# Kernel tuning notes

Measured on AMD Instinct MI355X. Metric: run time of the kernel, lower is better.

## Reference

```python
import jax, jax.numpy as jnp
import numpy as np

HEADS = 4
BN_EPS = 1e-5


def _linear_attention(x, heads):
    # x: [B, L, C]; per-head linear attention: softmax(Q,dim=feat) @ (softmax(K,dim=seq)^T @ V)
    B, L, C = x.shape
    dh = C // heads
    h = x.reshape(B, L, heads, dh)
    q = jax.nn.softmax(h, axis=-1)          # softmax over feature dim (dim=2 in torch)
    k = jax.nn.softmax(h, axis=1)           # softmax over sequence dim (dim=1 in torch)
    kv = jnp.einsum('blhd,blhe->bhde', k, h)   # [B, H, dh, dh]
    out = jnp.einsum('blhd,bhde->blhe', q, kv) # [B, L, H, dh]
    return out.reshape(B, L, C)


def setup_inputs() -> dict:
    key = jax.random.key(0)
    ks = jax.random.split(key, 10)
    B, C, L, DOUT, NB = 32, 32, 16384, 10, 3
    s = 0.1
    return {
        'x': jax.random.normal(ks[0], (B, C, L), jnp.float32),
        'fcW1': jax.random.normal(ks[1], (NB, C, C), jnp.float32) * s,
        'fcb1': jax.random.normal(ks[2], (NB, C), jnp.float32) * s,
        'fcW2': jax.random.normal(ks[3], (NB, C, C), jnp.float32) * s,
        'fcb2': jax.random.normal(ks[4], (NB, C), jnp.float32) * s,
        'Wh': jax.random.normal(ks[5], (C, C), jnp.float32) * s,
        'bh': jax.random.normal(ks[6], (C,), jnp.float32) * s,
        'bn_gamma': jnp.ones((C,), jnp.float32),
        'bn_beta': jnp.zeros((C,), jnp.float32),
        'bn_mean': jnp.zeros((C,), jnp.float32),
        'bn_var': jnp.ones((C,), jnp.float32),
        'Wf': jax.random.normal(ks[7], (C, DOUT), jnp.float32) * s,
        'bf': jax.random.normal(ks[8], (DOUT,), jnp.float32) * s,
    }


def reference(x, fcW1, fcb1, fcW2, fcb2, Wh, bh, bn_gamma, bn_beta, bn_mean, bn_var, Wf, bf):
    gelu = lambda t: jax.nn.gelu(t, approximate=False)  # torch default GELU is exact erf
    h = jnp.transpose(x, (0, 2, 1))  # [B, C, L] -> [B, L, C]
    n_blocks = fcW1.shape[0]
    for i in range(n_blocks):
        h = _linear_attention(h, HEADS)
        h = gelu(h @ fcW1[i] + fcb1[i])
        h = gelu(h @ fcW2[i] + fcb2[i])
    pooled = jnp.mean(h, axis=1)  # AdaptiveAvgPool1d(1) over L -> [B, C]
    y = pooled @ Wh + bh
    y = (y - bn_mean) * jax.lax.rsqrt(bn_var + BN_EPS) * bn_gamma + bn_beta  # BatchNorm1d (eval)
    y = gelu(y)
    return y @ Wf + bf
```

## Files before the change

### kernel.cpp

```cpp
#include <hip/hip_runtime.h>
#include <cstddef>

#define B_ 32
#define C_ 32
#define L_ 16384
#define H_ 4
#define DH_ 8
#define NB_ 3
#define DOUT_ 10
#define SEG_ 256
#define S_ (L_/SEG_)

#define TILE 256
#define AST  40
#define OST  260

typedef _Float16 f16_t;
typedef _Float16 f16x2 __attribute__((ext_vector_type(2)));
typedef _Float16 f16x8 __attribute__((ext_vector_type(8)));
typedef float    f32x4 __attribute__((ext_vector_type(4)));

__device__ __forceinline__ float gelu_f(float x){
    const float z  = fabsf(x) * 0.70710678118654752440f;
    const float t  = __builtin_amdgcn_rcpf(fmaf(0.3275911f, z, 1.0f));
    const float e  = __expf(-z * z);
    float p = fmaf(t, 1.061405429f, -1.453152027f);
    p = fmaf(t, p, 1.421413741f);
    p = fmaf(t, p, -0.284496736f);
    p = fmaf(t, p, 0.254829592f);
    const float erfz = 1.0f - p * t * e;
    const float phi  = fmaf(copysignf(erfz, x), 0.5f, 0.5f);
    return x * phi;
}

__global__ __launch_bounds__(256) void stats_kernel(const float* __restrict__ h,
                                                    float* __restrict__ part){
    const int seg = blockIdx.x;
    const int hd  = blockIdx.y;
    const int b   = blockIdx.z;
    const int t   = threadIdx.x;
    const int d   = t >> 5;
    const int j   = t & 31;

    __shared__ float tile[8][SEG_];
    __shared__ float sm[8];

    const float* hb = h + (size_t)b * ((size_t)C_*L_) + (size_t)(hd*DH_)*L_ + (size_t)seg*SEG_;

    for (int f = t; f < 8*SEG_/4; f += 256){
        const int row = f >> 6;
        const int c4  = (f & 63) << 2;
        *(f32x4*)&tile[row][c4] = *(const f32x4*)&hb[(size_t)row*L_ + c4];
    }
    __syncthreads();

    float m = -INFINITY;
    #pragma unroll
    for (int i = 0; i < SEG_/32; i++) m = fmaxf(m, tile[d][j + 32*i]);
    m = fmaxf(m, __shfl_xor(m, 1));
    m = fmaxf(m, __shfl_xor(m, 2));
    m = fmaxf(m, __shfl_xor(m, 4));
    m = fmaxf(m, __shfl_xor(m, 8));
    m = fmaxf(m, __shfl_xor(m, 16));
    if (j == 0) sm[d] = m;
    const float m_d = m;

    float s = 0.0f;
    float kv[8];
    #pragma unroll
    for (int e = 0; e < 8; e++) kv[e] = 0.0f;
    #pragma unroll
    for (int i = 0; i < SEG_/32; i++){
        const int k = j + 32*i;
        const float ek = __expf(tile[d][k] - m_d);
        s += ek;
        #pragma unroll
        for (int e = 0; e < 8; e++) kv[e] = fmaf(ek, tile[e][k], kv[e]);
    }
    s += __shfl_xor(s, 1);  s += __shfl_xor(s, 2);  s += __shfl_xor(s, 4);
    s += __shfl_xor(s, 8);  s += __shfl_xor(s, 16);
    #pragma unroll
    for (int e = 0; e < 8; e++){
        kv[e] += __shfl_xor(kv[e], 1);  kv[e] += __shfl_xor(kv[e], 2);
        kv[e] += __shfl_xor(kv[e], 4);  kv[e] += __shfl_xor(kv[e], 8);
        kv[e] += __shfl_xor(kv[e], 16);
    }
    __syncthreads();

    float* po = part + (size_t)((b*H_ + hd)*S_ + seg) * 80;
    if (j == 0){
        po[8 + d] = s;
        #pragma unroll
        for (int e = 0; e < 8; e++) po[16 + d*8 + e] = kv[e];
    }
    if (t < 8) po[t] = sm[t];
}

__global__ __launch_bounds__(64) void merge_kernel(const float* __restrict__ part,
                                                   float* __restrict__ kvn){
    const int bh = blockIdx.x;
    const int t  = threadIdx.x;
    const int d  = t >> 3;
    const float* p = part + (size_t)bh * S_ * 80;
    float M = -INFINITY;
    for (int s2 = 0; s2 < S_; s2++) M = fmaxf(M, p[s2*80 + d]);
    float ssum = 0.0f, kvsum = 0.0f;
    for (int s2 = 0; s2 < S_; s2++){
        float sc = __expf(p[s2*80 + d] - M);
        ssum  += p[s2*80 + 8  + d] * sc;
        kvsum += p[s2*80 + 16 + t] * sc;
    }
    kvn[(size_t)bh*64 + t] = kvsum / ssum;
}

template<bool LAST>
__global__ __launch_bounds__(256)
__attribute__((amdgpu_waves_per_eu(3, 4)))
void block_kernel(const float* hin,
                  float* hout,
                  const float* __restrict__ kvn,
                  const float* __restrict__ W1,
                  const float* __restrict__ b1,
                  const float* __restrict__ W2,
                  const float* __restrict__ b2,
                  float* __restrict__ part_out,
                  float* __restrict__ pooled){
    __shared__ __align__(16) char uni[TILE*AST*2];
    f16_t* Ash = (f16_t*)uni;
    float* O16 = (float*)uni;
    __shared__ f16_t Bsh1[32*AST];
    __shared__ f16_t Bsh2[32*AST];
    __shared__ float sb1[32], sb2[32];
    __shared__ float pool[32];

    const int tid = threadIdx.x;
    const int b   = blockIdx.y;
    const int l0  = blockIdx.x * TILE;
    const int l   = l0 + tid;
    const size_t base = (size_t)b * ((size_t)C_*L_);
    const float* kv = kvn + (size_t)b * (H_*DH_*DH_);

    for (int i = tid; i < 1024; i += 256){
        const int k = i >> 5, n = i & 31;
        Bsh1[n*AST + k] = (f16_t)W1[i];
        Bsh2[n*AST + k] = (f16_t)W2[i];
    }
    if (tid < 32){ sb1[tid] = b1[tid]; sb2[tid] = b2[tid]; }
    if (LAST && tid < 32) pool[tid] = 0.0f;

    float h[32];
    #pragma unroll
    for (int c = 0; c < 32; c++) h[c] = hin[base + (size_t)c*L_ + l];

    float attn[32];
    #pragma unroll
    for (int hh = 0; hh < 4; hh++){
        float mq = h[hh*8];
        #pragma unroll
        for (int d2 = 1; d2 < 8; d2++) mq = fmaxf(mq, h[hh*8 + d2]);
        float es[8]; float qs = 0.f;
        #pragma unroll
        for (int d2 = 0; d2 < 8; d2++){ es[d2] = __expf(h[hh*8 + d2] - mq); qs += es[d2]; }
        const float inv = __builtin_amdgcn_rcpf(qs);
        #pragma unroll
        for (int e = 0; e < 8; e++){
            float a = 0.f;
            #pragma unroll
            for (int d2 = 0; d2 < 8; d2++) a += es[d2] * kv[hh*64 + d2*8 + e];
            attn[hh*8 + e] = a * inv;
        }
    }

    #pragma unroll
    for (int k2 = 0; k2 < 32; k2 += 2){
        f16x2 pr = { (f16_t)attn[k2], (f16_t)attn[k2+1] };
        *(f16x2*)&Ash[tid*AST + k2] = pr;
    }
    __syncthreads();

    const int wv   = tid >> 6;
    const int lane = tid & 63;
    const int lr   = lane & 15;
    const int lk   = lane >> 4;
    const f32x4 zero = {0.f, 0.f, 0.f, 0.f};

    f16x8 a[4], bw[2];
    f32x4 d[8];

    #pragma unroll
    for (int mt = 0; mt < 4; mt++)
        a[mt] = *(const f16x8*)&Ash[(wv*64 + mt*16 + lr)*AST + lk*8];
    #pragma unroll
    for (int nt = 0; nt < 2; nt++)
        bw[nt] = *(const f16x8*)&Bsh1[(nt*16 + lr)*AST + lk*8];
    #pragma unroll
    for (int nt = 0; nt < 2; nt++)
        #pragma unroll
        for (int mt = 0; mt < 4; mt++)
            d[nt*4+mt] = __builtin_amdgcn_mfma_f32_16x16x32_f16(a[mt], bw[nt], zero, 0, 0, 0);

    #pragma unroll
    for (int nt = 0; nt < 2; nt++){
        const float bias = sb1[nt*16 + lr];
        #pragma unroll
        for (int mt = 0; mt < 4; mt++){
            #pragma unroll
            for (int r = 0; r < 4; r++){
                const float v = gelu_f(d[nt*4+mt][r] + bias);
                Ash[(wv*64 + mt*16 + lk*4 + r)*AST + (nt*16 + lr)] = (f16_t)v;
            }
        }
    }
    __syncthreads();

    #pragma unroll
    for (int mt = 0; mt < 4; mt++)
        a[mt] = *(const f16x8*)&Ash[(wv*64 + mt*16 + lr)*AST + lk*8];
    #pragma unroll
    for (int nt = 0; nt < 2; nt++)
        bw[nt] = *(const f16x8*)&Bsh2[(nt*16 + lr)*AST + lk*8];
    #pragma unroll
    for (int nt = 0; nt < 2; nt++)
        #pragma unroll
        for (int mt = 0; mt < 4; mt++)
            d[nt*4+mt] = __builtin_amdgcn_mfma_f32_16x16x32_f16(a[mt], bw[nt], zero, 0, 0, 0);

    #pragma unroll
    for (int nt = 0; nt < 2; nt++){
        const float bias = sb2[nt*16 + lr];
        #pragma unroll
        for (int mt = 0; mt < 4; mt++)
            #pragma unroll
            for (int r = 0; r < 4; r++)
                d[nt*4+mt][r] = gelu_f(d[nt*4+mt][r] + bias);
    }

    if (!LAST){
        const int row16 = tid >> 4;
        const int grp   = tid & 15;
        #pragma unroll
        for (int nt = 0; nt < 2; nt++){
            __syncthreads();
            #pragma unroll
            for (int mt = 0; mt < 4; mt++)
                *(f32x4*)&O16[lr*OST + wv*64 + mt*16 + lk*4] = d[nt*4+mt];
            __syncthreads();
            #pragma unroll
            for (int c = 0; c < 16; c++)
                hout[base + (size_t)(nt*16 + c)*L_ + l0 + tid] = O16[c*OST + tid];

            const int head = nt*2 + (row16 >> 3);
            const int dd   = row16 & 7;
            const float* rowD = &O16[row16*OST];
            const float* rowE = &O16[(row16 & 8)*OST];
            float m = -INFINITY;
            #pragma unroll
            for (int i = 0; i < 16; i++) m = fmaxf(m, rowD[grp + 16*i]);
            m = fmaxf(m, __shfl_xor(m, 1)); m = fmaxf(m, __shfl_xor(m, 2));
            m = fmaxf(m, __shfl_xor(m, 4)); m = fmaxf(m, __shfl_xor(m, 8));
            float s = 0.f, kvp[8];
            #pragma unroll
            for (int e = 0; e < 8; e++) kvp[e] = 0.f;
            #pragma unroll
            for (int i = 0; i < 16; i++){
                const int k = grp + 16*i;
                const float ek = __expf(rowD[k] - m);
                s += ek;
                #pragma unroll
                for (int e = 0; e < 8; e++) kvp[e] = fmaf(ek, rowE[e*OST + k], kvp[e]);
            }
            s += __shfl_xor(s, 1); s += __shfl_xor(s, 2);
            s += __shfl_xor(s, 4); s += __shfl_xor(s, 8);
            #pragma unroll
            for (int e = 0; e < 8; e++){
                kvp[e] += __shfl_xor(kvp[e], 1); kvp[e] += __shfl_xor(kvp[e], 2);
                kvp[e] += __shfl_xor(kvp[e], 4); kvp[e] += __shfl_xor(kvp[e], 8);
            }
            if (grp == 0){
                float* po = part_out + (size_t)((b*H_ + head)*S_ + blockIdx.x) * 80;
                po[dd]     = m;
                po[8 + dd] = s;
                #pragma unroll
                for (int e = 0; e < 8; e++) po[16 + dd*8 + e] = kvp[e];
            }
        }
    } else {
        __syncthreads();
        #pragma unroll
        for (int nt = 0; nt < 2; nt++){
            float ps = 0.f;
            #pragma unroll
            for (int mt = 0; mt < 4; mt++)
                ps += d[nt*4+mt][0] + d[nt*4+mt][1] + d[nt*4+mt][2] + d[nt*4+mt][3];
            atomicAdd(&pool[nt*16 + lr], ps);
        }
        __syncthreads();
        if (tid < 32) atomicAdd(&pooled[b*32 + tid], pool[tid]);
    }
}

__global__ __launch_bounds__(1024) void head_kernel(const float* __restrict__ pooled,
                                                    const float* __restrict__ Wh,
                                                    const float* __restrict__ bh,
                                                    const float* __restrict__ gam,
                                                    const float* __restrict__ bet,
                                                    const float* __restrict__ mean,
                                                    const float* __restrict__ var,
                                                    const float* __restrict__ Wf,
                                                    const float* __restrict__ bf,
                                                    float* __restrict__ out){
    __shared__ float y2[32][32];
    const int t = threadIdx.x;
    const int b = t >> 5, c = t & 31;
    float a = bh[c];
    const float invL = 1.0f / (float)L_;
    #pragma unroll
    for (int d = 0; d < 32; d++) a += (pooled[b*32 + d] * invL) * Wh[d*32 + c];
    a = (a - mean[c]) * rsqrtf(var[c] + 1e-5f) * gam[c] + bet[c];
    y2[b][c] = gelu_f(a);
    __syncthreads();
    if (t < B_*DOUT_){
        const int b2 = t / DOUT_, j = t % DOUT_;
        float r = bf[j];
        #pragma unroll
        for (int c2 = 0; c2 < 32; c2++) r += y2[b2][c2] * Wf[c2*DOUT_ + j];
        out[t] = r;
    }
}

extern "C" void kernel_launch(void* const* d_in, const int* in_sizes, int n_in,
                              void* d_out, int out_size, void* d_ws, size_t ws_size,
                              hipStream_t stream){
    (void)in_sizes; (void)n_in; (void)out_size; (void)ws_size;
    const float* x    = (const float*)d_in[0];
    const float* fW1  = (const float*)d_in[1];
    const float* fb1  = (const float*)d_in[2];
    const float* fW2  = (const float*)d_in[3];
    const float* fb2  = (const float*)d_in[4];
    const float* Wh   = (const float*)d_in[5];
    const float* bh   = (const float*)d_in[6];
    const float* gam  = (const float*)d_in[7];
    const float* bet  = (const float*)d_in[8];
    const float* mean = (const float*)d_in[9];
    const float* var  = (const float*)d_in[10];
    const float* Wf   = (const float*)d_in[11];
    const float* bf   = (const float*)d_in[12];
    float* out = (float*)d_out;

    float* hbuf   = (float*)d_ws;
    float* part   = hbuf + (size_t)B_*C_*L_;
    float* kvn    = part + (size_t)B_*H_*S_*80;
    float* pooled = kvn  + (size_t)B_*H_*64;

    hipMemsetAsync(pooled, 0, B_*C_*sizeof(float), stream);

    dim3 sgrid(S_, H_, B_);
    dim3 bgrid(L_/TILE, B_);

    stats_kernel<<<sgrid, 256, 0, stream>>>(x, part);
    merge_kernel<<<B_*H_, 64, 0, stream>>>(part, kvn);
    block_kernel<false><<<bgrid, 256, 0, stream>>>(x, hbuf, kvn,
        fW1, fb1, fW2, fb2, part, nullptr);
    merge_kernel<<<B_*H_, 64, 0, stream>>>(part, kvn);
    block_kernel<false><<<bgrid, 256, 0, stream>>>(hbuf, hbuf, kvn,
        fW1 + C_*C_, fb1 + C_, fW2 + C_*C_, fb2 + C_, part, nullptr);
    merge_kernel<<<B_*H_, 64, 0, stream>>>(part, kvn);
    block_kernel<true><<<bgrid, 256, 0, stream>>>(hbuf, nullptr, kvn,
        fW1 + 2*C_*C_, fb1 + 2*C_, fW2 + 2*C_*C_, fb2 + 2*C_, nullptr, pooled);

    head_kernel<<<1, 1024, 0, stream>>>(pooled, Wh, bh, gam, bet, mean, var, Wf, bf, out);
}
```

Before: 304.9 us.

## Fuse partial-stat merge into block kernel and double-buffer partials

```diff
diff --git a/kernel.cpp b/kernel.cpp
--- a/kernel.cpp
+++ b/kernel.cpp
@@ -34,13 +34,18 @@
 }
 
 __global__ __launch_bounds__(256) void stats_kernel(const float* __restrict__ h,
-                                                    float* __restrict__ part){
+                                                    float* __restrict__ part,
+                                                    float* __restrict__ pooled){
     const int seg = blockIdx.x;
     const int hd  = blockIdx.y;
     const int b   = blockIdx.z;
     const int t   = threadIdx.x;
     const int d   = t >> 5;
     const int j   = t & 31;
+
+    if (seg == 0 && hd == 0 && b == 0){
+        for (int i = t; i < B_*C_; i += 256) pooled[i] = 0.0f;
+    }
 
     __shared__ float tile[8][SEG_];
     __shared__ float sm[8];
@@ -96,29 +101,12 @@
     if (t < 8) po[t] = sm[t];
 }
 
-__global__ __launch_bounds__(64) void merge_kernel(const float* __restrict__ part,
-                                                   float* __restrict__ kvn){
-    const int bh = blockIdx.x;
-    const int t  = threadIdx.x;
-    const int d  = t >> 3;
-    const float* p = part + (size_t)bh * S_ * 80;
-    float M = -INFINITY;
-    for (int s2 = 0; s2 < S_; s2++) M = fmaxf(M, p[s2*80 + d]);
-    float ssum = 0.0f, kvsum = 0.0f;
-    for (int s2 = 0; s2 < S_; s2++){
-        float sc = __expf(p[s2*80 + d] - M);
-        ssum  += p[s2*80 + 8  + d] * sc;
-        kvsum += p[s2*80 + 16 + t] * sc;
-    }
-    kvn[(size_t)bh*64 + t] = kvsum / ssum;
-}
-
 template<bool LAST>
 __global__ __launch_bounds__(256)
-__attribute__((amdgpu_waves_per_eu(3, 4)))
+__attribute__((amdgpu_waves_per_eu(3, 8)))
 void block_kernel(const float* hin,
                   float* hout,
-                  const float* __restrict__ kvn,
+                  const float* __restrict__ part_in,
                   const float* __restrict__ W1,
                   const float* __restrict__ b1,
                   const float* __restrict__ W2,
@@ -131,6 +119,7 @@
     __shared__ f16_t Bsh1[32*AST];
     __shared__ f16_t Bsh2[32*AST];
     __shared__ float sb1[32], sb2[32];
+    __shared__ float skv[256];
     __shared__ float pool[32];
 
     const int tid = threadIdx.x;
@@ -138,7 +127,6 @@
     const int l0  = blockIdx.x * TILE;
     const int l   = l0 + tid;
     const size_t base = (size_t)b * ((size_t)C_*L_);
-    const float* kv = kvn + (size_t)b * (H_*DH_*DH_);
 
     for (int i = tid; i < 1024; i += 256){
         const int k = i >> 5, n = i & 31;
@@ -148,6 +136,25 @@
     if (tid < 32){ sb1[tid] = b1[tid]; sb2[tid] = b2[tid]; }
     if (LAST && tid < 32) pool[tid] = 0.0f;
 
+    {
+        const int head = tid >> 6;
+        const int de   = tid & 63;
+        const int dd   = de >> 3;
+        const float* p = part_in + (size_t)(b*H_ + head) * S_ * 80;
+        float M = -INFINITY;
+        #pragma unroll 4
+        for (int s2 = 0; s2 < S_; s2++) M = fmaxf(M, p[s2*80 + dd]);
+        float ssum = 0.f, kvsum = 0.f;
+        #pragma unroll 4
+        for (int s2 = 0; s2 < S_; s2++){
+            const float sc = __expf(p[s2*80 + dd] - M);
+            ssum  = fmaf(p[s2*80 + 8 + dd], sc, ssum);
+            kvsum = fmaf(p[s2*80 + 16 + de], sc, kvsum);
+        }
+        skv[head*64 + de] = kvsum * __builtin_amdgcn_rcpf(ssum);
+    }
+    __syncthreads();
+
     float h[32];
     #pragma unroll
     for (int c = 0; c < 32; c++) h[c] = hin[base + (size_t)c*L_ + l];
@@ -166,7 +173,7 @@
         for (int e = 0; e < 8; e++){
             float a = 0.f;
             #pragma unroll
-            for (int d2 = 0; d2 < 8; d2++) a += es[d2] * kv[hh*64 + d2*8 + e];
+            for (int d2 = 0; d2 < 8; d2++) a += es[d2] * skv[hh*64 + d2*8 + e];
             attn[hh*8 + e] = a * inv;
         }
     }
@@ -348,25 +355,19 @@
     float* out = (float*)d_out;
 
     float* hbuf   = (float*)d_ws;
-    float* part   = hbuf + (size_t)B_*C_*L_;
-    float* kvn    = part + (size_t)B_*H_*S_*80;
-    float* pooled = kvn  + (size_t)B_*H_*64;
-
-    hipMemsetAsync(pooled, 0, B_*C_*sizeof(float), stream);
+    float* partA  = hbuf  + (size_t)B_*C_*L_;
+    float* partB  = partA + (size_t)B_*H_*S_*80;
+    float* pooled = partB + (size_t)B_*H_*S_*80;
 
     dim3 sgrid(S_, H_, B_);
     dim3 bgrid(L_/TILE, B_);
 
-    stats_kernel<<<sgrid, 256, 0, stream>>>(x, part);
-    merge_kernel<<<B_*H_, 64, 0, stream>>>(part, kvn);
-    block_kernel<false><<<bgrid, 256, 0, stream>>>(x, hbuf, kvn,
-        fW1, fb1, fW2, fb2, part, nullptr);
-    merge_kernel<<<B_*H_, 64, 0, stream>>>(part, kvn);
-    block_kernel<false><<<bgrid, 256, 0, stream>>>(hbuf, hbuf, kvn,
-        fW1 + C_*C_, fb1 + C_, fW2 + C_*C_, fb2 + C_, part, nullptr);
-    merge_kernel<<<B_*H_, 64, 0, stream>>>(part, kvn);
-    block_kernel<true><<<bgrid, 256, 0, stream>>>(hbuf, nullptr, kvn,
+    stats_kernel<<<sgrid, 256, 0, stream>>>(x, partA, pooled);
+    block_kernel<false><<<bgrid, 256, 0, stream>>>(x, hbuf, partA,
+        fW1, fb1, fW2, fb2, partB, nullptr);
+    block_kernel<false><<<bgrid, 256, 0, stream>>>(hbuf, hbuf, partB,
+        fW1 + C_*C_, fb1 + C_, fW2 + C_*C_, fb2 + C_, partA, nullptr);
+    block_kernel<true><<<bgrid, 256, 0, stream>>>(hbuf, nullptr, partA,
         fW1 + 2*C_*C_, fb1 + 2*C_, fW2 + 2*C_*C_, fb2 + 2*C_, nullptr, pooled);
-
     head_kernel<<<1, 1024, 0, stream>>>(pooled, Wh, bh, gam, bet, mean, var, Wf, bf, out);
 }
```

Measured after the change: 344.0 us. 1.13x slower.
